# Kernel tuning notes

Hardware: AMD Instinct MI355X
Metric: run time of the kernel (lower is better)

The kernel has to match this reference:

```python
import jax, jax.numpy as jnp
import numpy as np
from jax import lax

B, T, C = 64, 1024, 256


def setup_inputs() -> dict:
    key = jax.random.key(0)
    k1, k2 = jax.random.split(key)
    sequences = jax.random.normal(k1, (B, T, C), dtype=jnp.float32)
    transitions = jax.random.normal(k2, (C, C), dtype=jnp.float32)
    return {"sequences": sequences, "transitions": transitions}


def _viterbi_decode(sequences, transitions):
    # sequences: [B, T, C] unary scores; transitions: [C_prev, C_cur]
    num_classes = sequences.shape[-1]
    emissions = jnp.swapaxes(sequences, 0, 1)  # [T, B, C]

    def fwd_step(alpha, emit):
        # alpha: [B, C_prev]; emit: [B, C_cur]
        m = alpha[:, :, None] + transitions[None, :, :]  # [B, C_prev, C_cur]
        bp = jnp.argmax(m, axis=1).astype(jnp.int32)     # [B, C_cur] backpointers
        new_alpha = jnp.max(m, axis=1) + emit            # [B, C_cur]
        return new_alpha, bp

    alpha, bps = lax.scan(fwd_step, emissions[0], emissions[1:])  # bps: [T-1, B, C]
    last_tag = jnp.argmax(alpha, axis=-1).astype(jnp.int32)       # [B]

    def back_step(tag, bp):
        # tag: [B] tag at t+1; bp: [B, C] backpointers computed at step t+1
        prev = jnp.take_along_axis(bp, tag[:, None], axis=1)[:, 0]
        return prev, prev

    _, tags = lax.scan(back_step, last_tag, bps, reverse=True)  # [T-1, B]
    full = jnp.concatenate([tags, last_tag[None, :]], axis=0)   # [T, B]
    return jnp.swapaxes(full, 0, 1)  # [B, T]


def reference(sequences, transitions):
    # Inference path of CRF.call: viterbi decode + one-hot over num_classes.
    tags = _viterbi_decode(sequences, transitions)
    return jax.nn.one_hot(tags, sequences.shape[-1], dtype=sequences.dtype)
```

## Files before the change

kernel.cpp:

```cpp
#include <hip/hip_runtime.h>

#define Bn 64
#define Tn 1024
#define Cn 256

#define FWD_SYNC()                                  \
  do {                                              \
    __builtin_amdgcn_sched_barrier(0);              \
    __builtin_amdgcn_s_waitcnt(0xC07F);             \
    __builtin_amdgcn_s_barrier();                   \
    __builtin_amdgcn_sched_barrier(0);              \
  } while (0)

template<int CTRL>
__device__ __forceinline__ float dpp_mov_f(float x) {
  return __int_as_float(__builtin_amdgcn_update_dpp(0, __float_as_int(x), CTRL, 0xF, 0xF, true));
}
template<int CTRL>
__device__ __forceinline__ void max_stage(float& v) {
  const float pv = __int_as_float(__builtin_amdgcn_update_dpp(
      (int)0xFF800000, __float_as_int(v), CTRL, 0xF, 0xF, false));
  v = fmaxf(v, pv);
}

__device__ __forceinline__ int argmax64_fast(float v, int i) {
  float mv = v;
  max_stage<0x111>(mv);
  max_stage<0x112>(mv);
  max_stage<0x114>(mv);
  max_stage<0x118>(mv);
  max_stage<0x142>(mv);
  max_stage<0x143>(mv);
  const float smax = __int_as_float(__builtin_amdgcn_readlane(__float_as_int(mv), 63));
  const unsigned long long m = __ballot(v == smax);
  const int ln = __ffsll((unsigned long long)m) - 1;
  return __builtin_amdgcn_readlane(i, ln);
}

__device__ __forceinline__ int apad(int m) { return (m >> 2) * 20 + (m & 3) * 4; }

__global__ __launch_bounds__(1024) void crf_fwd_kernel(
    float* __restrict__ seq, const float* __restrict__ trans,
    float* __restrict__ transT, int useT) {
  __shared__ float lds[64 * 65];
  const int bi = blockIdx.x;
  const int tid = threadIdx.x;

  if (bi < Bn) {
    float* sb = seq + (size_t)bi * (Tn * Cn);
    const int l = tid & 63;
    const int w = tid >> 6;
    const int c = l & 15;
    const int g = l >> 4;
    const int ccb = w * 16 + g * 4;
    const int cpb = c * 16;
    float4 tr4[16];
#pragma unroll
    for (int k = 0; k < 16; ++k)
      tr4[k] = *(const float4*)(trans + (size_t)(cpb + k) * Cn + ccb);

    float* ab0 = lds;
    float* ab1 = lds + 320;
    if (tid < 64) *(float4*)(ab0 + apad(tid)) = ((const float4*)sb)[tid];
    const bool leader = (c == 0);
    const int woff = apad(w * 4 + g);
    float4 e4, pna;
    if (leader) e4 = *(const float4*)(sb + Cn + ccb);
    FWD_SYNC();

    for (int t = 1; t < Tn; ++t) {
      float4 pf;
      if (leader) {
        if (t > 1) *(float4*)(sb + (size_t)(t - 1) * Cn + ccb) = pna;
        const int tn = (t + 1 < Tn) ? (t + 1) : (Tn - 1);
        pf = *(const float4*)(sb + (size_t)tn * Cn + ccb);
      }
      const float* av = (t & 1) ? ab0 : ab1;
      float* aw = (t & 1) ? ab1 : ab0;
      const float* avc = av + c * 20;
      float m0 = -__builtin_inff(), m1 = m0, m2 = m0, m3 = m0;
#pragma unroll
      for (int j = 0; j < 4; ++j) {
        const float4 a = *(const float4*)(avc + j * 4);
        float4 t0 = tr4[4 * j + 0];
        m0 = fmaxf(m0, a.x + t0.x); m1 = fmaxf(m1, a.x + t0.y);
        m2 = fmaxf(m2, a.x + t0.z); m3 = fmaxf(m3, a.x + t0.w);
        float4 t1 = tr4[4 * j + 1];
        m0 = fmaxf(m0, a.y + t1.x); m1 = fmaxf(m1, a.y + t1.y);
        m2 = fmaxf(m2, a.y + t1.z); m3 = fmaxf(m3, a.y + t1.w);
        float4 t2 = tr4[4 * j + 2];
        m0 = fmaxf(m0, a.z + t2.x); m1 = fmaxf(m1, a.z + t2.y);
        m2 = fmaxf(m2, a.z + t2.z); m3 = fmaxf(m3, a.z + t2.w);
        float4 t3 = tr4[4 * j + 3];
        m0 = fmaxf(m0, a.w + t3.x); m1 = fmaxf(m1, a.w + t3.y);
        m2 = fmaxf(m2, a.w + t3.z); m3 = fmaxf(m3, a.w + t3.w);
      }
      m0 = fmaxf(m0, dpp_mov_f<0x128>(m0)); m1 = fmaxf(m1, dpp_mov_f<0x128>(m1));
      m2 = fmaxf(m2, dpp_mov_f<0x128>(m2)); m3 = fmaxf(m3, dpp_mov_f<0x128>(m3));
      m0 = fmaxf(m0, dpp_mov_f<0x124>(m0)); m1 = fmaxf(m1, dpp_mov_f<0x124>(m1));
      m2 = fmaxf(m2, dpp_mov_f<0x124>(m2)); m3 = fmaxf(m3, dpp_mov_f<0x124>(m3));
      m0 = fmaxf(m0, dpp_mov_f<0x122>(m0)); m1 = fmaxf(m1, dpp_mov_f<0x122>(m1));
      m2 = fmaxf(m2, dpp_mov_f<0x122>(m2)); m3 = fmaxf(m3, dpp_mov_f<0x122>(m3));
      m0 = fmaxf(m0, dpp_mov_f<0x121>(m0)); m1 = fmaxf(m1, dpp_mov_f<0x121>(m1));
      m2 = fmaxf(m2, dpp_mov_f<0x121>(m2)); m3 = fmaxf(m3, dpp_mov_f<0x121>(m3));
      if (leader) {
        float4 na;
        na.x = m0 + e4.x; na.y = m1 + e4.y; na.z = m2 + e4.z; na.w = m3 + e4.w;
        *(float4*)(aw + woff) = na;
        pna = na;
        e4 = pf;
      }
      FWD_SYNC();
    }
    if (leader) *(float4*)(sb + (size_t)(Tn - 1) * Cn + ccb) = pna;
  } else if (useT) {
    const int idx = bi - Bn;
    const int ti = idx >> 2, tj = idx & 3;
    const int tx = tid & 63, ty = tid >> 6;
#pragma unroll
    for (int q = 0; q < 4; ++q) {
      const int row = q * 16 + ty;
      lds[tx * 65 + row] = trans[(size_t)(ti * 64 + row) * Cn + tj * 64 + tx];
    }
    __syncthreads();
#pragma unroll
    for (int q = 0; q < 4; ++q) {
      const int row = q * 16 + ty;
      transT[(size_t)(tj * 64 + row) * Cn + ti * 64 + tx] = lds[row * 65 + tx];
    }
  }
}

__device__ __forceinline__ float4 onehot4(int tg, int cp0) {
  float4 z;
  z.x = (tg == cp0 + 0) ? 1.0f : 0.0f; z.y = (tg == cp0 + 1) ? 1.0f : 0.0f;
  z.z = (tg == cp0 + 2) ? 1.0f : 0.0f; z.w = (tg == cp0 + 3) ? 1.0f : 0.0f;
  return z;
}

template<int K>
__device__ __forceinline__ int chain_chunk(
    const float* __restrict__ A, int* __restrict__ tags,
    const float* __restrict__ transT, int tag, int l) {
  const int cp0 = l * 4;
#pragma unroll
  for (int k = 0; k < K; ++k) {
    const float4 tv = *(const float4*)(transT + (size_t)tag * Cn + cp0);
    const float4 ac = *(const float4*)(A + k * Cn + cp0);
    float v = ac.x + tv.x; int i = cp0;
    float vv; bool cnd;
    vv = ac.y + tv.y; cnd = vv > v; v = cnd ? vv : v; i = cnd ? cp0 + 1 : i;
    vv = ac.z + tv.z; cnd = vv > v; v = cnd ? vv : v; i = cnd ? cp0 + 2 : i;
    vv = ac.w + tv.w; cnd = vv > v; v = cnd ? vv : v; i = cnd ? cp0 + 3 : i;
    tag = argmax64_fast(v, i);
    if (l == 0) tags[k] = tag;
  }
  return tag;
}

__global__ __launch_bounds__(256) void crf_bwd_kernel(
    const float* __restrict__ seq, const float* __restrict__ trans,
    const float* __restrict__ transT, float* __restrict__ out, int useT) {
  __shared__ float aL[2][16][Cn];
  __shared__ int tagL[2][16];
  const int b = blockIdx.x;
  const int tid = threadIdx.x;
  const int wv = tid >> 6;
  const int l = tid & 63;
  const int cp0 = l * 4;
  const float* sb = seq + (size_t)b * (Tn * Cn);
  float* ob = out + (size_t)b * (Tn * Cn);

  if (!useT) {
    if (wv == 0) {
      float4 a = *(const float4*)(sb + (size_t)(Tn - 1) * Cn + cp0);
      float v = a.x; int i = cp0; bool cnd;
      cnd = a.y > v; v = cnd ? a.y : v; i = cnd ? cp0 + 1 : i;
      cnd = a.z > v; v = cnd ? a.z : v; i = cnd ? cp0 + 2 : i;
      cnd = a.w > v; v = cnd ? a.w : v; i = cnd ? cp0 + 3 : i;
      int tag = argmax64_fast(v, i);
      *(float4*)(ob + (size_t)(Tn - 1) * Cn + cp0) = onehot4(tag, cp0);
      for (int t = Tn - 2; t >= 0; --t) {
        const float4 ac = *(const float4*)(sb + (size_t)t * Cn + cp0);
        float4 tv;
        tv.x = trans[(size_t)(cp0 + 0) * Cn + tag];
        tv.y = trans[(size_t)(cp0 + 1) * Cn + tag];
        tv.z = trans[(size_t)(cp0 + 2) * Cn + tag];
        tv.w = trans[(size_t)(cp0 + 3) * Cn + tag];
        float v2 = ac.x + tv.x; int i2 = cp0; float vv; bool c2;
        vv = ac.y + tv.y; c2 = vv > v2; v2 = c2 ? vv : v2; i2 = c2 ? cp0 + 1 : i2;
        vv = ac.z + tv.z; c2 = vv > v2; v2 = c2 ? vv : v2; i2 = c2 ? cp0 + 2 : i2;
        vv = ac.w + tv.w; c2 = vv > v2; v2 = c2 ? vv : v2; i2 = c2 ? cp0 + 3 : i2;
        tag = argmax64_fast(v2, i2);
        *(float4*)(ob + (size_t)t * Cn + cp0) = onehot4(tag, cp0);
      }
    }
    return;
  }

  int tag = 0;
  if (wv == 0) {
    float4 a = *(const float4*)(sb + (size_t)(Tn - 1) * Cn + cp0);
    float v = a.x; int i = cp0; bool cnd;
    cnd = a.y > v; v = cnd ? a.y : v; i = cnd ? cp0 + 1 : i;
    cnd = a.z > v; v = cnd ? a.z : v; i = cnd ? cp0 + 2 : i;
    cnd = a.w > v; v = cnd ? a.w : v; i = cnd ? cp0 + 3 : i;
    tag = argmax64_fast(v, i);
    *(float4*)(ob + (size_t)(Tn - 1) * Cn + cp0) = onehot4(tag, cp0);
  } else if (wv <= 2) {
    const int s0 = (wv == 1) ? 0 : 8, s1 = (wv == 1) ? 8 : 15;
    for (int s = s0; s < s1; ++s)
      *(float4*)(&aL[0][s][cp0]) = *(const float4*)(sb + (size_t)(1022 - s) * Cn + cp0);
  }
  __syncthreads();

  int p = 0, t0 = 1022, K = 15, pt0 = 0, pK = 0;
  for (int ch = 0; ch < 64; ++ch) {
    const int nt0 = t0 - K;
    if (wv == 0) {
      if (ch == 0) tag = chain_chunk<15>(&aL[p][0][0], tagL[p], transT, tag, l);
      else        tag = chain_chunk<16>(&aL[p][0][0], tagL[p], transT, tag, l);
    } else if (wv <= 2) {
      if (ch < 63) {
        const int s0 = (wv == 1) ? 0 : 8, s1 = (wv == 1) ? 8 : 16;
        for (int s = s0; s < s1; ++s)
          *(float4*)(&aL[1 - p][s][cp0]) =
              *(const float4*)(sb + (size_t)(nt0 - s) * Cn + cp0);
      }
    } else {
      if (ch > 0) {
        for (int k = 0; k < pK; ++k)
          *(float4*)(ob + (size_t)(pt0 - k) * Cn + cp0) =
              onehot4(tagL[1 - p][k], cp0);
      }
    }
    __syncthreads();
    pt0 = t0; pK = K; t0 = nt0; K = 16; p ^= 1;
  }
  if (wv == 3) {
    for (int k = 0; k < 16; ++k)
      *(float4*)(ob + (size_t)(15 - k) * Cn + cp0) = onehot4(tagL[1][k], cp0);
  }
}

extern "C" void kernel_launch(void* const* d_in, const int* in_sizes, int n_in,
                              void* d_out, int out_size, void* d_ws, size_t ws_size,
                              hipStream_t stream) {
  float* seq = (float*)d_in[0];
  const float* trans = (const float*)d_in[1];
  float* out = (float*)d_out;
  float* transT = (float*)d_ws;
  const int useT = (ws_size >= (size_t)Cn * Cn * sizeof(float)) ? 1 : 0;

  crf_fwd_kernel<<<dim3(Bn + 16), dim3(1024), 0, stream>>>(seq, trans, transT, useT);
  crf_bwd_kernel<<<dim3(Bn), dim3(256), 0, stream>>>(seq, trans, transT, out, useT);
}
```

Baseline: 1.309 ms.

## Process two batch sequences per forward block to amortize barriers

Each forward block now runs the Viterbi recurrence for two batch elements at once. The elements have separate double-buffered alpha arrays in LDS but share the register-resident transition tiles, so there is one barrier per timestep for both. The goal is to spread the per-step barrier and latency overhead across twice the work and give the compute units more independent instructions to interleave. In exchange the grid launches half as many forward blocks, 32 instead of 64 on a GPU with many CUs, so parallelism drops and each block's serial critical path roughly doubles its work.

```diff
diff --git a/kernel.cpp b/kernel.cpp
--- a/kernel.cpp
+++ b/kernel.cpp
@@ -39,6 +39,44 @@
 
 __device__ __forceinline__ int apad(int m) { return (m >> 2) * 20 + (m & 3) * 4; }
 
+__device__ __forceinline__ void fwd_step_batch(
+    const float* __restrict__ avc, float* __restrict__ aw, int woff,
+    const float4* __restrict__ tr4, bool leader,
+    float4& e4, float4& pna, float4 pf) {
+  float m0 = -__builtin_inff(), m1 = m0, m2 = m0, m3 = m0;
+#pragma unroll
+  for (int j = 0; j < 4; ++j) {
+    const float4 a = *(const float4*)(avc + j * 4);
+    float4 t0 = tr4[4 * j + 0];
+    m0 = fmaxf(m0, a.x + t0.x); m1 = fmaxf(m1, a.x + t0.y);
+    m2 = fmaxf(m2, a.x + t0.z); m3 = fmaxf(m3, a.x + t0.w);
+    float4 t1 = tr4[4 * j + 1];
+    m0 = fmaxf(m0, a.y + t1.x); m1 = fmaxf(m1, a.y + t1.y);
+    m2 = fmaxf(m2, a.y + t1.z); m3 = fmaxf(m3, a.y + t1.w);
+    float4 t2 = tr4[4 * j + 2];
+    m0 = fmaxf(m0, a.z + t2.x); m1 = fmaxf(m1, a.z + t2.y);
+    m2 = fmaxf(m2, a.z + t2.z); m3 = fmaxf(m3, a.z + t2.w);
+    float4 t3 = tr4[4 * j + 3];
+    m0 = fmaxf(m0, a.w + t3.x); m1 = fmaxf(m1, a.w + t3.y);
+    m2 = fmaxf(m2, a.w + t3.z); m3 = fmaxf(m3, a.w + t3.w);
+  }
+  m0 = fmaxf(m0, dpp_mov_f<0x128>(m0)); m1 = fmaxf(m1, dpp_mov_f<0x128>(m1));
+  m2 = fmaxf(m2, dpp_mov_f<0x128>(m2)); m3 = fmaxf(m3, dpp_mov_f<0x128>(m3));
+  m0 = fmaxf(m0, dpp_mov_f<0x124>(m0)); m1 = fmaxf(m1, dpp_mov_f<0x124>(m1));
+  m2 = fmaxf(m2, dpp_mov_f<0x124>(m2)); m3 = fmaxf(m3, dpp_mov_f<0x124>(m3));
+  m0 = fmaxf(m0, dpp_mov_f<0x122>(m0)); m1 = fmaxf(m1, dpp_mov_f<0x122>(m1));
+  m2 = fmaxf(m2, dpp_mov_f<0x122>(m2)); m3 = fmaxf(m3, dpp_mov_f<0x122>(m3));
+  m0 = fmaxf(m0, dpp_mov_f<0x121>(m0)); m1 = fmaxf(m1, dpp_mov_f<0x121>(m1));
+  m2 = fmaxf(m2, dpp_mov_f<0x121>(m2)); m3 = fmaxf(m3, dpp_mov_f<0x121>(m3));
+  if (leader) {
+    float4 na;
+    na.x = m0 + e4.x; na.y = m1 + e4.y; na.z = m2 + e4.z; na.w = m3 + e4.w;
+    *(float4*)(aw + woff) = na;
+    pna = na;
+    e4 = pf;
+  }
+}
+
 __global__ __launch_bounds__(1024) void crf_fwd_kernel(
     float* __restrict__ seq, const float* __restrict__ trans,
     float* __restrict__ transT, int useT) {
@@ -46,8 +84,9 @@
   const int bi = blockIdx.x;
   const int tid = threadIdx.x;
 
-  if (bi < Bn) {
-    float* sb = seq + (size_t)bi * (Tn * Cn);
+  if (bi < Bn / 2) {
+    float* sbA = seq + (size_t)(2 * bi) * (Tn * Cn);
+    float* sbB = seq + (size_t)(2 * bi + 1) * (Tn * Cn);
     const int l = tid & 63;
     const int w = tid >> 6;
     const int c = l & 15;
@@ -59,62 +98,45 @@
     for (int k = 0; k < 16; ++k)
       tr4[k] = *(const float4*)(trans + (size_t)(cpb + k) * Cn + ccb);
 
-    float* ab0 = lds;
-    float* ab1 = lds + 320;
-    if (tid < 64) *(float4*)(ab0 + apad(tid)) = ((const float4*)sb)[tid];
+    float* abA0 = lds;        float* abA1 = lds + 320;
+    float* abB0 = lds + 640;  float* abB1 = lds + 960;
+    if (tid < 64) *(float4*)(abA0 + apad(tid)) = ((const float4*)sbA)[tid];
+    else if (tid < 128) *(float4*)(abB0 + apad(tid - 64)) = ((const float4*)sbB)[tid - 64];
     const bool leader = (c == 0);
     const int woff = apad(w * 4 + g);
-    float4 e4, pna;
-    if (leader) e4 = *(const float4*)(sb + Cn + ccb);
+    float4 e4A, pnaA, e4B, pnaB;
+    if (leader) {
+      e4A = *(const float4*)(sbA + Cn + ccb);
+      e4B = *(const float4*)(sbB + Cn + ccb);
+    }
     FWD_SYNC();
 
     for (int t = 1; t < Tn; ++t) {
-      float4 pf;
+      float4 pfA, pfB;
       if (leader) {
-        if (t > 1) *(float4*)(sb + (size_t)(t - 1) * Cn + ccb) = pna;
+        if (t > 1) {
+          *(float4*)(sbA + (size_t)(t - 1) * Cn + ccb) = pnaA;
+          *(float4*)(sbB + (size_t)(t - 1) * Cn + ccb) = pnaB;
+        }
         const int tn = (t + 1 < Tn) ? (t + 1) : (Tn - 1);
-        pf = *(const float4*)(sb + (size_t)tn * Cn + ccb);
-      }
-      const float* av = (t & 1) ? ab0 : ab1;
-      float* aw = (t & 1) ? ab1 : ab0;
-      const float* avc = av + c * 20;
-      float m0 = -__builtin_inff(), m1 = m0, m2 = m0, m3 = m0;
-#pragma unroll
-      for (int j = 0; j < 4; ++j) {
-        const float4 a = *(const float4*)(avc + j * 4);
-        float4 t0 = tr4[4 * j + 0];
-        m0 = fmaxf(m0, a.x + t0.x); m1 = fmaxf(m1, a.x + t0.y);
-        m2 = fmaxf(m2, a.x + t0.z); m3 = fmaxf(m3, a.x + t0.w);
-        float4 t1 = tr4[4 * j + 1];
-        m0 = fmaxf(m0, a.y + t1.x); m1 = fmaxf(m1, a.y + t1.y);
-        m2 = fmaxf(m2, a.y + t1.z); m3 = fmaxf(m3, a.y + t1.w);
-        float4 t2 = tr4[4 * j + 2];
-        m0 = fmaxf(m0, a.z + t2.x); m1 = fmaxf(m1, a.z + t2.y);
-        m2 = fmaxf(m2, a.z + t2.z); m3 = fmaxf(m3, a.z + t2.w);
-        float4 t3 = tr4[4 * j + 3];
-        m0 = fmaxf(m0, a.w + t3.x); m1 = fmaxf(m1, a.w + t3.y);
-        m2 = fmaxf(m2, a.w + t3.z); m3 = fmaxf(m3, a.w + t3.w);
-      }
-      m0 = fmaxf(m0, dpp_mov_f<0x128>(m0)); m1 = fmaxf(m1, dpp_mov_f<0x128>(m1));
-      m2 = fmaxf(m2, dpp_mov_f<0x128>(m2)); m3 = fmaxf(m3, dpp_mov_f<0x128>(m3));
-      m0 = fmaxf(m0, dpp_mov_f<0x124>(m0)); m1 = fmaxf(m1, dpp_mov_f<0x124>(m1));
-      m2 = fmaxf(m2, dpp_mov_f<0x124>(m2)); m3 = fmaxf(m3, dpp_mov_f<0x124>(m3));
-      m0 = fmaxf(m0, dpp_mov_f<0x122>(m0)); m1 = fmaxf(m1, dpp_mov_f<0x122>(m1));
-      m2 = fmaxf(m2, dpp_mov_f<0x122>(m2)); m3 = fmaxf(m3, dpp_mov_f<0x122>(m3));
-      m0 = fmaxf(m0, dpp_mov_f<0x121>(m0)); m1 = fmaxf(m1, dpp_mov_f<0x121>(m1));
-      m2 = fmaxf(m2, dpp_mov_f<0x121>(m2)); m3 = fmaxf(m3, dpp_mov_f<0x121>(m3));
-      if (leader) {
-        float4 na;
-        na.x = m0 + e4.x; na.y = m1 + e4.y; na.z = m2 + e4.z; na.w = m3 + e4.w;
-        *(float4*)(aw + woff) = na;
-        pna = na;
-        e4 = pf;
-      }
+        pfA = *(const float4*)(sbA + (size_t)tn * Cn + ccb);
+        pfB = *(const float4*)(sbB + (size_t)tn * Cn + ccb);
+      }
+      const int par = t & 1;
+      const float* avA = par ? abA0 : abA1;
+      float* awA = par ? abA1 : abA0;
+      const float* avB = par ? abB0 : abB1;
+      float* awB = par ? abB1 : abB0;
+      fwd_step_batch(avA + c * 20, awA, woff, tr4, leader, e4A, pnaA, pfA);
+      fwd_step_batch(avB + c * 20, awB, woff, tr4, leader, e4B, pnaB, pfB);
       FWD_SYNC();
     }
-    if (leader) *(float4*)(sb + (size_t)(Tn - 1) * Cn + ccb) = pna;
+    if (leader) {
+      *(float4*)(sbA + (size_t)(Tn - 1) * Cn + ccb) = pnaA;
+      *(float4*)(sbB + (size_t)(Tn - 1) * Cn + ccb) = pnaB;
+    }
   } else if (useT) {
-    const int idx = bi - Bn;
+    const int idx = bi - Bn / 2;
     const int ti = idx >> 2, tj = idx & 3;
     const int tx = tid & 63, ty = tid >> 6;
 #pragma unroll
@@ -252,6 +274,6 @@
   float* transT = (float*)d_ws;
   const int useT = (ws_size >= (size_t)Cn * Cn * sizeof(float)) ? 1 : 0;
 
-  crf_fwd_kernel<<<dim3(Bn + 16), dim3(1024), 0, stream>>>(seq, trans, transT, useT);
+  crf_fwd_kernel<<<dim3(Bn / 2 + 16), dim3(1024), 0, stream>>>(seq, trans, transT, useT);
   crf_bwd_kernel<<<dim3(Bn), dim3(256), 0, stream>>>(seq, trans, transT, out, useT);
 }
```

New measurement: 2.508 ms. +91.6%, slower.
